# Performance work log

Measured on AMD Instinct MI355X. Metric: run time of the kernel, lower is better.

## Reference

```python
import jax, jax.numpy as jnp
import numpy as np

B, N_CITY, EC, VOCAB = 4096, 50, 128, 40000


def setup_inputs() -> dict:
    key = jax.random.key(0)
    k1, k2, k3, k4 = jax.random.split(key, 4)
    x = jax.random.normal(k1, (B, EC), dtype=jnp.float32)
    top_city_emb = jax.random.normal(k2, (B, N_CITY, EC), dtype=jnp.float32)
    top_city_id = jax.random.randint(k3, (B, N_CITY), 0, VOCAB)
    prob = jnp.zeros((B, VOCAB), dtype=jnp.float32)
    # nn.Linear(EC, EC) params
    W = jax.random.normal(k4, (EC, EC), dtype=jnp.float32) * (1.0 / np.sqrt(EC))
    b = jnp.zeros((EC,), dtype=jnp.float32)
    return {"x": x, "top_city_emb": top_city_emb, "top_city_id": top_city_id,
            "prob": prob, "W": W, "b": b}


def reference(x, top_city_emb, top_city_id, prob, W, b):
    # Linear projection (torch Linear: x @ W^T + b)
    emb_pred = x @ W.T + b                                  # [B, EC]
    # Broadcast dot-product score against candidate embeddings
    scores = jnp.einsum('be,bne->bn', emb_pred, top_city_emb)  # [B, N_CITY]
    p = jax.nn.softmax(scores, axis=1)                      # [B, N_CITY]
    # Scatter-add softmax probs into the vocab-sized output
    rows = jnp.arange(p.shape[0])[:, None]                  # [B, 1] -> broadcast to [B, N_CITY]
    rows = jnp.broadcast_to(rows, top_city_id.shape)
    out = jnp.zeros_like(prob).at[rows, top_city_id].add(p) + 1e-6
    return out
```

## Files before the change

### kernel.cpp

```cpp
#include <hip/hip_runtime.h>
#include <hip/hip_bf16.h>

#define NC    50
#define EC    128
#define VOCAB 40000

__global__ __launch_bounds__(256)
void EmbDotSoftMax_wtpack_kernel(const float* __restrict__ W,
                                 float4*      __restrict__ WTp)
{
    const int t = threadIdx.x;
    #pragma unroll
    for (int idx = t; idx < (EC / 4) * EC; idx += 256) {
        const int k4 = idx >> 7;
        const int e  = idx & 127;
        WTp[idx] = reinterpret_cast<const float4*>(W)[e * (EC / 4) + k4];
    }
}

__global__ __launch_bounds__(128)
void EmbDotSoftMax_scatter_kernel(const float*  __restrict__ x,
                                  const float*  __restrict__ emb,
                                  const int*    __restrict__ ids,
                                  const float4* __restrict__ WTp,
                                  const float*  __restrict__ bias,
                                  float*        __restrict__ out)
{
    const int b   = blockIdx.x;
    const int tid = threadIdx.x;

    __shared__ float4 x_s4[EC / 4];
    __shared__ float  pred_s[EC];
    __shared__ float  score_s[NC];

    float* out_row = out + (size_t)b * VOCAB;

    if (tid < EC / 4)
        x_s4[tid] = reinterpret_cast<const float4*>(x + (size_t)b * EC)[tid];
    __syncthreads();

    {
        float acc = 0.0f;
        #pragma unroll
        for (int k4 = 0; k4 < EC / 4; ++k4) {
            const float4 w  = WTp[k4 * EC + tid];
            const float4 xv = x_s4[k4];
            acc = fmaf(w.x, xv.x, acc);
            acc = fmaf(w.y, xv.y, acc);
            acc = fmaf(w.z, xv.z, acc);
            acc = fmaf(w.w, xv.w, acc);
        }
        pred_s[tid] = acc + bias[tid];
    }
    __syncthreads();

    {
        const int w = tid >> 6;
        const int l = tid & 63;
        if (l < NC / 2) {
            const int n = w * (NC / 2) + l;
            const float4* er =
                reinterpret_cast<const float4*>(emb + ((size_t)b * NC + n) * EC);
            float acc = 0.0f;
            #pragma unroll
            for (int j = 0; j < EC / 4; ++j) {
                const float4 e4 = er[j];
                const float4 p4 = reinterpret_cast<const float4*>(pred_s)[j];
                acc = fmaf(e4.x, p4.x, acc);
                acc = fmaf(e4.y, p4.y, acc);
                acc = fmaf(e4.z, p4.z, acc);
                acc = fmaf(e4.w, p4.w, acc);
            }
            score_s[n] = acc;
        }
    }
    __syncthreads();

    if (tid < NC) {
        float m = -1e30f;
        #pragma unroll
        for (int n = 0; n < NC; ++n) m = fmaxf(m, score_s[n]);
        float sum = 0.0f;
        #pragma unroll
        for (int n = 0; n < NC; ++n) sum += __expf(score_s[n] - m);
        const float p  = __expf(score_s[tid] - m) / sum;
        const int   id = ids[(size_t)b * NC + tid];
        atomicAdd(out_row + id, p);
    }
}

__global__ __launch_bounds__(128)
void EmbDotSoftMax_scatter_fb(const float* __restrict__ x,
                              const float* __restrict__ emb,
                              const int*   __restrict__ ids,
                              const float* __restrict__ W,
                              const float* __restrict__ bias,
                              float*       __restrict__ out)
{
    const int b   = blockIdx.x;
    const int tid = threadIdx.x;
    const int w   = tid >> 6;
    const int l   = tid & 63;
    __shared__ float pred_s[EC];
    __shared__ float scores_s[NC];
    float* out_row = out + (size_t)b * VOCAB;
    {
        const float x0 = x[(size_t)b * EC + l];
        const float x1 = x[(size_t)b * EC + 64 + l];
        const float* Wbase = W + (size_t)w * 64 * EC;
        float mine = 0.0f;
        #pragma unroll 8
        for (int i = 0; i < 64; ++i) {
            const float* row = Wbase + i * EC;
            float part = fmaf(x0, row[l], x1 * row[l + 64]);
            #pragma unroll
            for (int off = 32; off; off >>= 1)
                part += __shfl_xor(part, off);
            if (i == l) mine = part;
        }
        pred_s[w * 64 + l] = mine + bias[w * 64 + l];
    }
    __syncthreads();
    {
        const float p0 = pred_s[l];
        const float p1 = pred_s[l + 64];
        const float* base = emb + (size_t)b * NC * EC + (size_t)w * (NC / 2) * EC;
        float part[NC / 2];
        #pragma unroll
        for (int i = 0; i < NC / 2; ++i) {
            const float* er = base + i * EC;
            part[i] = fmaf(p0, er[l], p1 * er[l + 64]);
        }
        #pragma unroll
        for (int off = 32; off; off >>= 1) {
            #pragma unroll
            for (int i = 0; i < NC / 2; ++i)
                part[i] += __shfl_xor(part[i], off);
        }
        if (l == 0) {
            #pragma unroll
            for (int i = 0; i < NC / 2; ++i)
                scores_s[w * (NC / 2) + i] = part[i];
        }
    }
    __syncthreads();
    if (tid < NC) {
        float m = -1e30f;
        #pragma unroll
        for (int n = 0; n < NC; ++n) m = fmaxf(m, scores_s[n]);
        float sum = 0.0f;
        #pragma unroll
        for (int n = 0; n < NC; ++n) sum += __expf(scores_s[n] - m);
        const float p = __expf(scores_s[tid] - m) / sum;
        atomicAdd(out_row + ids[(size_t)b * NC + tid], p);
    }
}

extern "C" void kernel_launch(void* const* d_in, const int* in_sizes, int n_in,
                              void* d_out, int out_size, void* d_ws, size_t ws_size,
                              hipStream_t stream) {
    const float* x    = (const float*)d_in[0];
    const float* emb  = (const float*)d_in[1];
    const int*   ids  = (const int*)d_in[2];
    const float* W    = (const float*)d_in[4];
    const float* bias = (const float*)d_in[5];
    float*       out  = (float*)d_out;

    const int B = in_sizes[0] / EC;
    const size_t ws_needed = (size_t)(EC / 4) * EC * sizeof(float4);

    hipMemsetAsync(d_out, 0, (size_t)out_size * sizeof(float), stream);

    if (ws_size >= ws_needed) {
        float4* WTp = (float4*)d_ws;
        hipLaunchKernelGGL(EmbDotSoftMax_wtpack_kernel,
                           dim3(1), dim3(256), 0, stream, W, WTp);
        hipLaunchKernelGGL(EmbDotSoftMax_scatter_kernel,
                           dim3(B), dim3(128), 0, stream,
                           x, emb, ids, WTp, bias, out);
    } else {
        hipLaunchKernelGGL(EmbDotSoftMax_scatter_fb,
                           dim3(B), dim3(128), 0, stream,
                           x, emb, ids, W, bias, out);
    }
}
```

Measured before the change: 171.2 us.

## Fuse output initialisation into scatter kernel and replace atomics with deduplicated stores

Drops the separate memset of the vocab-sized output. Each block now fills its own output row with the 1e-6 epsilon using float4 stores, then writes the softmax probabilities. Duplicate city ids within a row are merged in shared memory, so each distinct id gets one plain store instead of an atomicAdd. This saves one full-tensor write pass and the atomics, and it also adds the epsilon that was missing before. In exchange, each block does extra store work, and there is a small O(NC^2) dedup loop.

Measured after the change: 189.0 us. 1.1x slower.

```diff
diff --git a/kernel.cpp b/kernel.cpp
--- a/kernel.cpp
+++ b/kernel.cpp
@@ -19,12 +19,12 @@
 }
 
 __global__ __launch_bounds__(128)
-void EmbDotSoftMax_scatter_kernel(const float*  __restrict__ x,
-                                  const float*  __restrict__ emb,
-                                  const int*    __restrict__ ids,
-                                  const float4* __restrict__ WTp,
-                                  const float*  __restrict__ bias,
-                                  float*        __restrict__ out)
+void EmbDotSoftMax_fused_kernel(const float*  __restrict__ x,
+                                const float*  __restrict__ emb,
+                                const int*    __restrict__ ids,
+                                const float4* __restrict__ WTp,
+                                const float*  __restrict__ bias,
+                                float*        __restrict__ out)
 {
     const int b   = blockIdx.x;
     const int tid = threadIdx.x;
@@ -32,11 +32,22 @@
     __shared__ float4 x_s4[EC / 4];
     __shared__ float  pred_s[EC];
     __shared__ float  score_s[NC];
+    __shared__ float  p_s[NC];
+    __shared__ int    id_s[NC];
 
     float* out_row = out + (size_t)b * VOCAB;
+
+    {
+        const float4 fv = make_float4(1e-6f, 1e-6f, 1e-6f, 1e-6f);
+        float4* out4 = reinterpret_cast<float4*>(out_row);
+        for (int i = tid; i < VOCAB / 4; i += 128)
+            out4[i] = fv;
+    }
 
     if (tid < EC / 4)
         x_s4[tid] = reinterpret_cast<const float4*>(x + (size_t)b * EC)[tid];
+    if (tid < NC)
+        id_s[tid] = ids[(size_t)b * NC + tid];
     __syncthreads();
 
     {
@@ -83,9 +94,23 @@
         float sum = 0.0f;
         #pragma unroll
         for (int n = 0; n < NC; ++n) sum += __expf(score_s[n] - m);
-        const float p  = __expf(score_s[tid] - m) / sum;
-        const int   id = ids[(size_t)b * NC + tid];
-        atomicAdd(out_row + id, p);
+        p_s[tid] = __expf(score_s[tid] - m) / sum;
+    }
+    __syncthreads();
+
+    if (tid < NC) {
+        const int myid = id_s[tid];
+        int   first = -1;
+        float s     = 0.0f;
+        #pragma unroll
+        for (int j = 0; j < NC; ++j) {
+            if (id_s[j] == myid) {
+                if (first < 0) first = j;
+                s += p_s[j];
+            }
+        }
+        if (first == tid)
+            out_row[myid] = s + 1e-6f;
     }
 }
 
@@ -169,16 +194,15 @@
     const int B = in_sizes[0] / EC;
     const size_t ws_needed = (size_t)(EC / 4) * EC * sizeof(float4);
 
-    hipMemsetAsync(d_out, 0, (size_t)out_size * sizeof(float), stream);
-
     if (ws_size >= ws_needed) {
         float4* WTp = (float4*)d_ws;
         hipLaunchKernelGGL(EmbDotSoftMax_wtpack_kernel,
                            dim3(1), dim3(256), 0, stream, W, WTp);
-        hipLaunchKernelGGL(EmbDotSoftMax_scatter_kernel,
+        hipLaunchKernelGGL(EmbDotSoftMax_fused_kernel,
                            dim3(B), dim3(128), 0, stream,
                            x, emb, ids, WTp, bias, out);
     } else {
+        hipMemsetAsync(d_out, 0, (size_t)out_size * sizeof(float), stream);
         hipLaunchKernelGGL(EmbDotSoftMax_scatter_fb,
                            dim3(B), dim3(128), 0, stream,
                            x, emb, ids, W, bias, out);
```

## Build each output row in LDS and stream it out, replacing the memset

Applied to the files above, without the earlier changes.

Replaces the per-row kernel and the separate output memset with a persistent kernel. Each block handles 8 rows and keeps a full vocab-sized row in LDS, initialised to 1e-6. For each row it scatters the softmax probabilities into LDS, writes the whole row to global memory with float4 stores, then resets only the touched entries. This folds the zero-fill, the +1e-6 epsilon and the scatter into one write pass and removes the global atomics. In exchange the ~160KB LDS footprint limits occupancy to one block per CU, and the row work is serialised inside each block. The W transpose-pack kernel also moves from one block to 16.

New measurement: 312.7 us. 1.83x slower.

```diff
diff --git a/kernel.cpp b/kernel.cpp
--- a/kernel.cpp
+++ b/kernel.cpp
@@ -1,66 +1,76 @@
 #include <hip/hip_runtime.h>
 #include <hip/hip_bf16.h>
 
-#define NC    50
-#define EC    128
+#define NC   50
+#define EC   128
 #define VOCAB 40000
+#define RPB  8
 
 __global__ __launch_bounds__(256)
 void EmbDotSoftMax_wtpack_kernel(const float* __restrict__ W,
                                  float4*      __restrict__ WTp)
 {
-    const int t = threadIdx.x;
-    #pragma unroll
-    for (int idx = t; idx < (EC / 4) * EC; idx += 256) {
+    const int idx = blockIdx.x * 256 + threadIdx.x;
+    if (idx < (EC / 4) * EC) {
         const int k4 = idx >> 7;
         const int e  = idx & 127;
         WTp[idx] = reinterpret_cast<const float4*>(W)[e * (EC / 4) + k4];
     }
 }
 
-__global__ __launch_bounds__(128)
-void EmbDotSoftMax_scatter_kernel(const float*  __restrict__ x,
+__global__ __launch_bounds__(256)
+void EmbDotSoftMax_persist_kernel(const float*  __restrict__ x,
                                   const float*  __restrict__ emb,
                                   const int*    __restrict__ ids,
                                   const float4* __restrict__ WTp,
                                   const float*  __restrict__ bias,
                                   float*        __restrict__ out)
 {
-    const int b   = blockIdx.x;
-    const int tid = threadIdx.x;
-
+    __shared__ float  lds_row[VOCAB];
     __shared__ float4 x_s4[EC / 4];
     __shared__ float  pred_s[EC];
     __shared__ float  score_s[NC];
-
-    float* out_row = out + (size_t)b * VOCAB;
-
-    if (tid < EC / 4)
-        x_s4[tid] = reinterpret_cast<const float4*>(x + (size_t)b * EC)[tid];
-    __syncthreads();
+    __shared__ int    id_s[NC];
+
+    const int tid  = threadIdx.x;
+    const int base = blockIdx.x * RPB;
 
     {
-        float acc = 0.0f;
-        #pragma unroll
-        for (int k4 = 0; k4 < EC / 4; ++k4) {
-            const float4 w  = WTp[k4 * EC + tid];
-            const float4 xv = x_s4[k4];
-            acc = fmaf(w.x, xv.x, acc);
-            acc = fmaf(w.y, xv.y, acc);
-            acc = fmaf(w.z, xv.z, acc);
-            acc = fmaf(w.w, xv.w, acc);
-        }
-        pred_s[tid] = acc + bias[tid];
-    }
-    __syncthreads();
-
-    {
-        const int w = tid >> 6;
-        const int l = tid & 63;
-        if (l < NC / 2) {
-            const int n = w * (NC / 2) + l;
+        const float4 fv = make_float4(1e-6f, 1e-6f, 1e-6f, 1e-6f);
+        float4* lr4 = reinterpret_cast<float4*>(lds_row);
+        for (int j = tid; j < VOCAB / 4; j += 256) lr4[j] = fv;
+    }
+
+    for (int i = 0; i < RPB; ++i) {
+        const int r = base + i;
+
+        int prev_id = -1;
+        if (i > 0 && tid < NC) prev_id = id_s[tid];
+
+        if (tid < EC / 4)
+            x_s4[tid] = reinterpret_cast<const float4*>(x + (size_t)r * EC)[tid];
+        if (tid < NC)
+            id_s[tid] = ids[(size_t)r * NC + tid];
+        __syncthreads();
+
+        if (tid < EC) {
+            float acc = 0.0f;
+            #pragma unroll
+            for (int k4 = 0; k4 < EC / 4; ++k4) {
+                const float4 w  = WTp[k4 * EC + tid];
+                const float4 xv = x_s4[k4];
+                acc = fmaf(w.x, xv.x, acc);
+                acc = fmaf(w.y, xv.y, acc);
+                acc = fmaf(w.z, xv.z, acc);
+                acc = fmaf(w.w, xv.w, acc);
+            }
+            pred_s[tid] = acc + bias[tid];
+        }
+        __syncthreads();
+
+        if (tid < NC) {
             const float4* er =
-                reinterpret_cast<const float4*>(emb + ((size_t)b * NC + n) * EC);
+                reinterpret_cast<const float4*>(emb + ((size_t)r * NC + tid) * EC);
             float acc = 0.0f;
             #pragma unroll
             for (int j = 0; j < EC / 4; ++j) {
@@ -71,21 +81,32 @@
                 acc = fmaf(e4.z, p4.z, acc);
                 acc = fmaf(e4.w, p4.w, acc);
             }
-            score_s[n] = acc;
-        }
-    }
-    __syncthreads();
-
-    if (tid < NC) {
-        float m = -1e30f;
-        #pragma unroll
-        for (int n = 0; n < NC; ++n) m = fmaxf(m, score_s[n]);
-        float sum = 0.0f;
-        #pragma unroll
-        for (int n = 0; n < NC; ++n) sum += __expf(score_s[n] - m);
-        const float p  = __expf(score_s[tid] - m) / sum;
-        const int   id = ids[(size_t)b * NC + tid];
-        atomicAdd(out_row + id, p);
+            score_s[tid] = acc;
+        }
+        __syncthreads();
+
+        float p = 0.0f;
+        if (tid < NC) {
+            float m = -1e30f;
+            #pragma unroll
+            for (int n = 0; n < NC; ++n) m = fmaxf(m, score_s[n]);
+            float sum = 0.0f;
+            #pragma unroll
+            for (int n = 0; n < NC; ++n) sum += __expf(score_s[n] - m);
+            p = __expf(score_s[tid] - m) / sum;
+        }
+
+        if (prev_id >= 0) lds_row[prev_id] = 1e-6f;
+        __syncthreads();
+        if (tid < NC) atomicAdd(&lds_row[id_s[tid]], p);
+        __syncthreads();
+
+        {
+            const float4* lr4 = reinterpret_cast<const float4*>(lds_row);
+            float4* orow = reinterpret_cast<float4*>(out + (size_t)r * VOCAB);
+            for (int j = tid; j < VOCAB / 4; j += 256)
+                orow[j] = lr4[j];
+        }
     }
 }
 
@@ -169,16 +190,15 @@
     const int B = in_sizes[0] / EC;
     const size_t ws_needed = (size_t)(EC / 4) * EC * sizeof(float4);
 
-    hipMemsetAsync(d_out, 0, (size_t)out_size * sizeof(float), stream);
-
-    if (ws_size >= ws_needed) {
+    if (ws_size >= ws_needed && (B % RPB) == 0) {
         float4* WTp = (float4*)d_ws;
         hipLaunchKernelGGL(EmbDotSoftMax_wtpack_kernel,
-                           dim3(1), dim3(256), 0, stream, W, WTp);
-        hipLaunchKernelGGL(EmbDotSoftMax_scatter_kernel,
-                           dim3(B), dim3(128), 0, stream,
+                           dim3(16), dim3(256), 0, stream, W, WTp);
+        hipLaunchKernelGGL(EmbDotSoftMax_persist_kernel,
+                           dim3(B / RPB), dim3(256), 0, stream,
                            x, emb, ids, WTp, bias, out);
     } else {
+        hipMemsetAsync(d_out, 0, (size_t)out_size * sizeof(float), stream);
         hipLaunchKernelGGL(EmbDotSoftMax_scatter_fb,
                            dim3(B), dim3(128), 0, stream,
                            x, emb, ids, W, bias, out);
```
